# Kernel tuning notes

Measured on AMD Instinct MI355X. Metric: run time of the kernel, lower is better.

## Reference

```python
import jax, jax.numpy as jnp
import numpy as np

PH, PW = 7, 7
SPATIAL_SCALE = 0.0625


def _hat_int(t):
    # Antiderivative of the unit hat (triangle) function phi(t)=max(0,1-|t|),
    # i.e. integral_{-inf}^{t} phi. Piecewise quadratic, saturates to [0,1].
    t = jnp.clip(t, -1.0, 1.0)
    return jnp.where(t <= 0, 0.5 * (t + 1.0) ** 2, 1.0 - 0.5 * (1.0 - t) ** 2)


def _bin_weights(lo, hi, size):
    # lo, hi: [R, P] continuous bin boundaries (in feature-map coordinates).
    # Returns [R, P, size]: exact 1D integral of the hat basis at each integer
    # grid node over [lo, hi]. Bilinear interpolation is the tensor product of
    # 1D hat bases, so the exact 2D PrRoI integral separates into these weights.
    grid = jnp.arange(size, dtype=lo.dtype)
    return _hat_int(hi[..., None] - grid) - _hat_int(lo[..., None] - grid)


def _prroi_pool(features, rois):
    N, C, H, W = features.shape
    R = rois.shape[0]
    dt = features.dtype
    bidx = rois[:, 0].astype(jnp.int32)
    x1 = rois[:, 1] * SPATIAL_SCALE
    y1 = rois[:, 2] * SPATIAL_SCALE
    x2 = rois[:, 3] * SPATIAL_SCALE
    y2 = rois[:, 4] * SPATIAL_SCALE
    roi_w = jnp.maximum(x2 - x1, 0.0)
    roi_h = jnp.maximum(y2 - y1, 0.0)
    bw = roi_w / PW  # [R]
    bh = roi_h / PH
    px = jnp.arange(PW, dtype=dt)
    py = jnp.arange(PH, dtype=dt)
    x_lo = x1[:, None] + px[None, :] * bw[:, None]  # [R, PW]
    x_hi = x_lo + bw[:, None]
    y_lo = y1[:, None] + py[None, :] * bh[:, None]  # [R, PH]
    y_hi = y_lo + bh[:, None]
    Wx = _bin_weights(x_lo, x_hi, W)  # [R, PW, W]
    Wy = _bin_weights(y_lo, y_hi, H)  # [R, PH, H]
    area = bw * bh  # [R]
    inv_area = jnp.where(area > 0, 1.0 / jnp.maximum(area, 1e-12), 0.0)
    out = jnp.zeros((R, C, PH, PW), dtype=dt)
    for n in range(N):  # small fixed batch loop; avoids [R,C,H,W] gather
        m = (bidx == n).astype(dt)
        out = out + jnp.einsum('rph,chw,rqw->rcpq', Wy * m[:, None, None], features[n], Wx)
    return out * inv_area[:, None, None, None]


def setup_inputs() -> dict:
    key = jax.random.key(0)
    k1, k2, k3, k4, k5, k6 = jax.random.split(key, 6)
    N, C, H, W, R = 2, 256, 152, 152, 512
    features = jax.random.normal(k1, (N, C, H, W), dtype=jnp.float32)
    img = H / SPATIAL_SCALE  # 2432 px image
    bidx = jax.random.randint(k2, (R,), 0, N).astype(jnp.float32)
    x1 = jax.random.uniform(k3, (R,), minval=0.0, maxval=img * 0.7)
    y1 = jax.random.uniform(k4, (R,), minval=0.0, maxval=img * 0.7)
    x2 = x1 + jax.random.uniform(k5, (R,), minval=32.0, maxval=img * 0.3)
    y2 = y1 + jax.random.uniform(k6, (R,), minval=32.0, maxval=img * 0.3)
    rois = jnp.stack([bidx, x1, y1, x2, y2], axis=1).astype(jnp.float32)
    return {"features": features, "rois": rois}


def reference(features, rois):
    return _prroi_pool(features, rois)
```

## Files before the change

kernel.cpp:

```cpp
#include <hip/hip_runtime.h>

#define PHH 7
#define PWW 7
#define WXW 48
static constexpr float SPATIAL_SCALE = 0.0625f;

__device__ __forceinline__ float hat_int(float t) {
    t = fminf(fmaxf(t, -1.0f), 1.0f);
    float a = t + 1.0f, b = 1.0f - t;
    return (t <= 0.0f) ? 0.5f * a * a : 1.0f - 0.5f * b * b;
}

__device__ __forceinline__ float bin_w(float lo, float hi, float g) {
    return hat_int(hi - g) - hat_int(lo - g);
}

__device__ __forceinline__ unsigned short f32_to_bf16_rne(float x) {
    unsigned int u = __float_as_uint(x);
    unsigned int r = 0x7FFFu + ((u >> 16) & 1u);
    return (unsigned short)((u + r) >> 16);
}

__device__ __forceinline__ float bf_lo(unsigned int v) {
    return __uint_as_float(v << 16);
}
__device__ __forceinline__ float bf_hi(unsigned int v) {
    return __uint_as_float(v & 0xFFFF0000u);
}

__global__ __launch_bounds__(256) void transpose_weights(
    const float* __restrict__ src, unsigned short* __restrict__ dst,
    const float* __restrict__ rois, float* __restrict__ wx,
    float* __restrict__ wys, int C, int HW, int H, int W, int R)
{
    const int bid = (int)blockIdx.x +
                    (int)gridDim.x * ((int)blockIdx.y + (int)gridDim.y * (int)blockIdx.z);
    const int tid = threadIdx.x;
    if (bid < R && tid < 112) {
        const float* roi = rois + (size_t)bid * 5;
        const float x1 = roi[1] * SPATIAL_SCALE;
        const float y1 = roi[2] * SPATIAL_SCALE;
        const float x2 = roi[3] * SPATIAL_SCALE;
        const float y2 = roi[4] * SPATIAL_SCALE;
        const float bw = fmaxf(x2 - x1, 0.0f) / (float)PWW;
        const float bh = fmaxf(y2 - y1, 0.0f) / (float)PHH;
        const float area = bw * bh;
        const float inv_area = (area > 0.0f) ? 1.0f / fmaxf(area, 1e-12f) : 0.0f;
        if (tid < WXW) {
            const int w0 = max(0, (int)ceilf(x1 - 1.0f));
            const int w1 = min(W - 1, (int)floorf(x2 + 1.0f));
            const int ww = min(w1 - w0 + 1, WXW);
            const float g = (float)(w0 + tid);
            float* o = wx + ((size_t)bid * WXW + tid) * 8;
            #pragma unroll
            for (int q = 0; q < PWW; ++q) {
                const float lo = x1 + (float)q * bw;
                o[q] = (tid < ww) ? bin_w(lo, lo + bw, g) * inv_area : 0.0f;
            }
            o[7] = 0.0f;
        }
        {
            const int p = tid >> 4;
            const int i = tid & 15;
            const float ylo = y1 + (float)p * bh;
            const float yhi = ylo + bh;
            const int h0 = max(0, (int)ceilf(ylo - 1.0f));
            const int h1 = min(H - 1, (int)floorf(yhi + 1.0f));
            const int nh = min(h1 - h0 + 1, 16);
            wys[((size_t)bid * PHH + p) * 16 + i] =
                (i < nh) ? bin_w(ylo, yhi, (float)(h0 + i)) : 0.0f;
        }
    }

    __shared__ unsigned short tile[64][66];
    const int n = blockIdx.z;
    const int hw0 = blockIdx.x * 64;
    const int c0 = blockIdx.y * 64;
    const float* s = src + (size_t)n * C * HW;
    unsigned short* d = dst + (size_t)n * C * HW;

    const int tx = threadIdx.x & 63;
    const int ty = threadIdx.x >> 6;
    #pragma unroll
    for (int i = 0; i < 16; ++i) {
        const int cl = ty * 16 + i;
        const int c = c0 + cl, hw = hw0 + tx;
        if (c < C && hw < HW)
            tile[cl][tx] = f32_to_bf16_rne(s[(size_t)c * HW + hw]);
    }
    __syncthreads();

    const int cl = threadIdx.x & 31;
    const int hb = threadIdx.x >> 5;
    #pragma unroll
    for (int i = 0; i < 8; ++i) {
        const int hwl = hb * 8 + i;
        const int hw = hw0 + hwl;
        const int c = c0 + 2 * cl;
        if (hw < HW && c < C) {
            const unsigned int v = (unsigned int)tile[2 * cl][hwl]
                                 | ((unsigned int)tile[2 * cl + 1][hwl] << 16);
            *(unsigned int*)(d + (size_t)hw * C + c) = v;
        }
    }
}

__global__ __launch_bounds__(128, 4) void prroi_pool_nolds(
    const unsigned short* __restrict__ ft,
    const float* __restrict__ rois,
    const float* __restrict__ wx,
    const float* __restrict__ wys,
    float* __restrict__ out,
    int H, int W, int R)
{
    const int nwg = R * PHH;
    int task = (int)blockIdx.x;
    if ((nwg & 7) == 0) {
        const int cpx = nwg >> 3;
        task = (task & 7) * cpx + (task >> 3);
    }
    const int r = task / PHH;
    const int p = task % PHH;

    const int chHalf = threadIdx.x >> 6;
    const int lane = threadIdx.x & 63;
    const int c0 = chHalf * 128 + lane * 2;

    const float* roi = rois + (size_t)r * 5;
    const int b = (int)roi[0];
    const float x1 = roi[1] * SPATIAL_SCALE;
    const float y1 = roi[2] * SPATIAL_SCALE;
    const float x2 = roi[3] * SPATIAL_SCALE;
    const float y2 = roi[4] * SPATIAL_SCALE;
    const float bh = fmaxf(y2 - y1, 0.0f) / (float)PHH;

    const float ylo = y1 + (float)p * bh;
    const float yhi = ylo + bh;
    const int h0 = max(0, (int)ceilf(ylo - 1.0f));
    const int h1 = min(H - 1, (int)floorf(yhi + 1.0f));
    const int w0 = max(0, (int)ceilf(x1 - 1.0f));
    const int w1 = min(W - 1, (int)floorf(x2 + 1.0f));
    const int nh = min(h1 - h0 + 1, 16);
    const int nh4 = (nh + 3) & ~3;
    const int ww = min(w1 - w0 + 1, WXW);

    const float* wysr = wys + ((size_t)r * PHH + p) * 16;
    const float* wxr = wx + (size_t)r * WXW * 8;

    float acc[PWW][2];
    #pragma unroll
    for (int q = 0; q < PWW; ++q) { acc[q][0] = 0.0f; acc[q][1] = 0.0f; }

    const size_t rowstride = (size_t)W * 256;
    const unsigned short* base =
        ft + ((size_t)b * H + (size_t)h0) * rowstride + (size_t)w0 * 256 + c0;
    const int nhm1 = nh - 1;

    for (int chunk = 0; chunk < ww; chunk += 8) {
        int off[8];
        #pragma unroll
        for (int j = 0; j < 8; ++j)
            off[j] = (chunk + j < ww) ? (chunk + j) * 256 : 0;

        float u[2][8];
        #pragma unroll
        for (int j = 0; j < 8; ++j) { u[0][j] = 0.0f; u[1][j] = 0.0f; }

        for (int i = 0; i < nh4; i += 4) {
            unsigned int v[4][8];
            #pragma unroll
            for (int k = 0; k < 4; ++k) {
                const unsigned short* rp = base + (size_t)min(i + k, nhm1) * rowstride;
                #pragma unroll
                for (int j = 0; j < 8; ++j)
                    v[k][j] = *(const unsigned int*)(rp + off[j]);
            }
            #pragma unroll
            for (int k = 0; k < 4; ++k) {
                const float wy = wysr[i + k];
                #pragma unroll
                for (int j = 0; j < 8; ++j) {
                    u[0][j] = fmaf(wy, bf_lo(v[k][j]), u[0][j]);
                    u[1][j] = fmaf(wy, bf_hi(v[k][j]), u[1][j]);
                }
            }
        }

        #pragma unroll
        for (int j = 0; j < 8; ++j) {
            const float4 wa = *(const float4*)&wxr[(chunk + j) * 8];
            const float4 wb = *(const float4*)&wxr[(chunk + j) * 8 + 4];
            acc[0][0] = fmaf(wa.x, u[0][j], acc[0][0]);
            acc[0][1] = fmaf(wa.x, u[1][j], acc[0][1]);
            acc[1][0] = fmaf(wa.y, u[0][j], acc[1][0]);
            acc[1][1] = fmaf(wa.y, u[1][j], acc[1][1]);
            acc[2][0] = fmaf(wa.z, u[0][j], acc[2][0]);
            acc[2][1] = fmaf(wa.z, u[1][j], acc[2][1]);
            acc[3][0] = fmaf(wa.w, u[0][j], acc[3][0]);
            acc[3][1] = fmaf(wa.w, u[1][j], acc[3][1]);
            acc[4][0] = fmaf(wb.x, u[0][j], acc[4][0]);
            acc[4][1] = fmaf(wb.x, u[1][j], acc[4][1]);
            acc[5][0] = fmaf(wb.y, u[0][j], acc[5][0]);
            acc[5][1] = fmaf(wb.y, u[1][j], acc[5][1]);
            acc[6][0] = fmaf(wb.z, u[0][j], acc[6][0]);
            acc[6][1] = fmaf(wb.z, u[1][j], acc[6][1]);
        }
    }

    float* o = out + ((size_t)r * 256 + c0) * (PHH * PWW) + p * PWW;
    #pragma unroll
    for (int q = 0; q < PWW; ++q) {
        o[q]             = acc[q][0];
        o[PHH * PWW + q] = acc[q][1];
    }
}

__global__ __launch_bounds__(256) void prroi_pool_nchw(
    const float* __restrict__ f, const float* __restrict__ rois,
    float* __restrict__ out, int C, int H, int W, int R)
{
    const int idx = blockIdx.x * blockDim.x + threadIdx.x;
    const int total = R * C * PHH * PWW;
    if (idx >= total) return;
    const int q = idx % PWW;
    const int p = (idx / PWW) % PHH;
    const int c = (idx / (PWW * PHH)) % C;
    const int r = idx / (PWW * PHH * C);
    const float* roi = rois + (size_t)r * 5;
    const int b = (int)roi[0];
    const float x1 = roi[1] * SPATIAL_SCALE;
    const float y1 = roi[2] * SPATIAL_SCALE;
    const float x2 = roi[3] * SPATIAL_SCALE;
    const float y2 = roi[4] * SPATIAL_SCALE;
    const float bw = fmaxf(x2 - x1, 0.0f) / (float)PWW;
    const float bh = fmaxf(y2 - y1, 0.0f) / (float)PHH;
    const float area = bw * bh;
    const float inv_area = (area > 0.0f) ? 1.0f / fmaxf(area, 1e-12f) : 0.0f;
    const float xlo = x1 + (float)q * bw, xhi = xlo + bw;
    const float ylo = y1 + (float)p * bh, yhi = ylo + bh;
    const int h0 = max(0, (int)ceilf(ylo - 1.0f));
    const int h1 = min(H - 1, (int)floorf(yhi + 1.0f));
    const int w0 = max(0, (int)ceilf(xlo - 1.0f));
    const int w1 = min(W - 1, (int)floorf(xhi + 1.0f));
    float acc = 0.0f;
    for (int h = h0; h <= h1; ++h) {
        const float wy = bin_w(ylo, yhi, (float)h);
        const float* fr = f + (((size_t)b * C + c) * H + h) * W;
        for (int w = w0; w <= w1; ++w)
            acc = fmaf(wy * bin_w(xlo, xhi, (float)w), fr[w], acc);
    }
    out[idx] = acc * inv_area;
}

extern "C" void kernel_launch(void* const* d_in, const int* in_sizes, int n_in,
                              void* d_out, int out_size, void* d_ws, size_t ws_size,
                              hipStream_t stream)
{
    const float* features = (const float*)d_in[0];
    const float* rois = (const float*)d_in[1];
    float* out = (float*)d_out;

    const int C = 256, H = 152, W = 152;
    const int N = in_sizes[0] / (C * H * W);
    const int R = in_sizes[1] / 5;

    const size_t ft_bytes = (size_t)N * C * H * W * sizeof(unsigned short);
    const size_t wx_off = ft_bytes;
    const size_t wys_off = wx_off + (size_t)R * WXW * 8 * 4;
    const size_t need = wys_off + (size_t)R * PHH * 16 * 4;

    if (ws_size >= need && C == 256) {
        unsigned short* ft = (unsigned short*)d_ws;
        float* wx = (float*)((char*)d_ws + wx_off);
        float* wys = (float*)((char*)d_ws + wys_off);
        const int HW = H * W;
        dim3 tgrid((HW + 63) / 64, (C + 63) / 64, N);
        transpose_weights<<<tgrid, 256, 0, stream>>>(
            features, ft, rois, wx, wys, C, HW, H, W, R);
        prroi_pool_nolds<<<R * PHH, 128, 0, stream>>>(ft, rois, wx, wys, out, H, W, R);
    } else {
        const int total = R * C * PHH * PWW;
        prroi_pool_nchw<<<(total + 255) / 256, 256, 0, stream>>>(features, rois, out, C, H, W, R);
    }
}
```

Measured before the change: 56.05 us.

## Stream feature tiles into LDS via async global_load_lds double buffering

Replaces the direct register loads of bf16 feature rows with direct global-to-LDS DMA loads into a per-wave double-buffered ring. The next 4x8 tile is issued before the current one is consumed, and explicit vmcnt waits let memory latency overlap the FMA work while cutting register pressure. It adds 32KB of shared memory per block and drops the occupancy hint, which may reduce resident blocks. Correctness depends on the hand-written vmcnt counting matching the number of issued loads, and on no barrier being needed because each wave only reads its own slab.

```diff
diff --git a/kernel.cpp b/kernel.cpp
--- a/kernel.cpp
+++ b/kernel.cpp
@@ -26,6 +26,13 @@
 }
 __device__ __forceinline__ float bf_hi(unsigned int v) {
     return __uint_as_float(v & 0xFFFF0000u);
+}
+
+__device__ __forceinline__ void gload_lds4(const unsigned short* g, void* lds) {
+    __builtin_amdgcn_global_load_lds(
+        (const __attribute__((address_space(1))) unsigned int*)g,
+        (__attribute__((address_space(3))) unsigned int*)lds,
+        4, 0, 0);
 }
 
 __global__ __launch_bounds__(256) void transpose_weights(
@@ -105,7 +112,7 @@
     }
 }
 
-__global__ __launch_bounds__(128, 4) void prroi_pool_nolds(
+__global__ __launch_bounds__(128) void prroi_pool_dma(
     const unsigned short* __restrict__ ft,
     const float* __restrict__ rois,
     const float* __restrict__ wx,
@@ -147,6 +154,9 @@
     const float* wysr = wys + ((size_t)r * PHH + p) * 16;
     const float* wxr = wx + (size_t)r * WXW * 8;
 
+    __shared__ unsigned int slab[2][2][2048];
+    unsigned int (*sl)[2048] = slab[chHalf];
+
     float acc[PWW][2];
     #pragma unroll
     for (int q = 0; q < PWW; ++q) { acc[q][0] = 0.0f; acc[q][1] = 0.0f; }
@@ -155,41 +165,57 @@
     const unsigned short* base =
         ft + ((size_t)b * H + (size_t)h0) * rowstride + (size_t)w0 * 256 + c0;
     const int nhm1 = nh - 1;
-
-    for (int chunk = 0; chunk < ww; chunk += 8) {
-        int off[8];
+    const int nchunks = (ww + 7) >> 3;
+    const int nrq = nh4 >> 2;
+    const int ntiles = nchunks * nrq;
+
+    auto issue = [&](int c, int rq, int ring) {
         #pragma unroll
-        for (int j = 0; j < 8; ++j)
-            off[j] = (chunk + j < ww) ? (chunk + j) * 256 : 0;
-
+        for (int k = 0; k < 4; ++k) {
+            const int row = min(rq * 4 + k, nhm1);
+            const unsigned short* rp = base + (size_t)row * rowstride;
+            #pragma unroll
+            for (int j = 0; j < 8; ++j) {
+                const int col = c * 8 + j;
+                const int off = (col < ww) ? col * 256 : 0;
+                gload_lds4(rp + off, &sl[ring][(k * 8 + j) * 64]);
+            }
+        }
+    };
+
+    issue(0, 0, 0);
+    int t = 0;
+    for (int c = 0; c < nchunks; ++c) {
         float u[2][8];
         #pragma unroll
         for (int j = 0; j < 8; ++j) { u[0][j] = 0.0f; u[1][j] = 0.0f; }
 
-        for (int i = 0; i < nh4; i += 4) {
-            unsigned int v[4][8];
-            #pragma unroll
-            for (int k = 0; k < 4; ++k) {
-                const unsigned short* rp = base + (size_t)min(i + k, nhm1) * rowstride;
-                #pragma unroll
-                for (int j = 0; j < 8; ++j)
-                    v[k][j] = *(const unsigned int*)(rp + off[j]);
+        for (int rq = 0; rq < nrq; ++rq, ++t) {
+            const int ring = t & 1;
+            if (t + 1 < ntiles) {
+                int cn = c, rqn = rq + 1;
+                if (rqn == nrq) { cn = c + 1; rqn = 0; }
+                issue(cn, rqn, (t + 1) & 1);
+                asm volatile("s_waitcnt vmcnt(32)" ::: "memory");
+            } else {
+                asm volatile("s_waitcnt vmcnt(0)" ::: "memory");
             }
             #pragma unroll
             for (int k = 0; k < 4; ++k) {
-                const float wy = wysr[i + k];
+                const float wy = wysr[rq * 4 + k];
                 #pragma unroll
                 for (int j = 0; j < 8; ++j) {
-                    u[0][j] = fmaf(wy, bf_lo(v[k][j]), u[0][j]);
-                    u[1][j] = fmaf(wy, bf_hi(v[k][j]), u[1][j]);
+                    const unsigned int v = sl[ring][(k * 8 + j) * 64 + lane];
+                    u[0][j] = fmaf(wy, bf_lo(v), u[0][j]);
+                    u[1][j] = fmaf(wy, bf_hi(v), u[1][j]);
                 }
             }
         }
 
         #pragma unroll
         for (int j = 0; j < 8; ++j) {
-            const float4 wa = *(const float4*)&wxr[(chunk + j) * 8];
-            const float4 wb = *(const float4*)&wxr[(chunk + j) * 8 + 4];
+            const float4 wa = *(const float4*)&wxr[(c * 8 + j) * 8];
+            const float4 wb = *(const float4*)&wxr[(c * 8 + j) * 8 + 4];
             acc[0][0] = fmaf(wa.x, u[0][j], acc[0][0]);
             acc[0][1] = fmaf(wa.x, u[1][j], acc[0][1]);
             acc[1][0] = fmaf(wa.y, u[0][j], acc[1][0]);
@@ -277,7 +303,7 @@
         dim3 tgrid((HW + 63) / 64, (C + 63) / 64, N);
         transpose_weights<<<tgrid, 256, 0, stream>>>(
             features, ft, rois, wx, wys, C, HW, H, W, R);
-        prroi_pool_nolds<<<R * PHH, 128, 0, stream>>>(ft, rois, wx, wys, out, H, W, R);
+        prroi_pool_dma<<<R * PHH, 128, 0, stream>>>(ft, rois, wx, wys, out, H, W, R);
     } else {
         const int total = R * C * PHH * PWW;
         prroi_pool_nchw<<<(total + 255) / 256, 256, 0, stream>>>(features, rois, out, C, H, W, R);
```

After: 70.19 us. 25.2% more time.

## Split column chunks across waves with 4-channel vector loads and LDS reduction

Applied to the files above, without the earlier changes.

Each thread now covers 4 channels with 8-byte loads instead of 2 channels with 4-byte loads, so one wave spans all 256 channels. The two waves of a block instead split the width chunks (alternating 8-column chunks) and combine their partial accumulators through shared memory before writing. This widens memory accesses and changes the parallel split, but it doubles register use for the accumulators and adds a sync plus an LDS reduction. Load imbalance between waves is possible when the number of columns is not a multiple of 16.

```diff
diff --git a/kernel.cpp b/kernel.cpp
--- a/kernel.cpp
+++ b/kernel.cpp
@@ -105,7 +105,7 @@
     }
 }
 
-__global__ __launch_bounds__(128, 4) void prroi_pool_nolds(
+__global__ __launch_bounds__(128, 4) void prroi_pool_u2(
     const unsigned short* __restrict__ ft,
     const float* __restrict__ rois,
     const float* __restrict__ wx,
@@ -122,9 +122,9 @@
     const int r = task / PHH;
     const int p = task % PHH;
 
-    const int chHalf = threadIdx.x >> 6;
+    const int colWave = threadIdx.x >> 6;
     const int lane = threadIdx.x & 63;
-    const int c0 = chHalf * 128 + lane * 2;
+    const int c0 = lane * 4;
 
     const float* roi = rois + (size_t)r * 5;
     const int b = (int)roi[0];
@@ -141,47 +141,55 @@
     const int w0 = max(0, (int)ceilf(x1 - 1.0f));
     const int w1 = min(W - 1, (int)floorf(x2 + 1.0f));
     const int nh = min(h1 - h0 + 1, 16);
-    const int nh4 = (nh + 3) & ~3;
+    const int nh2 = (nh + 1) & ~1;
     const int ww = min(w1 - w0 + 1, WXW);
 
     const float* wysr = wys + ((size_t)r * PHH + p) * 16;
     const float* wxr = wx + (size_t)r * WXW * 8;
 
-    float acc[PWW][2];
+    __shared__ float rbuf[64 * 29];
+
+    float acc[PWW][4];
     #pragma unroll
-    for (int q = 0; q < PWW; ++q) { acc[q][0] = 0.0f; acc[q][1] = 0.0f; }
+    for (int q = 0; q < PWW; ++q)
+        #pragma unroll
+        for (int ch = 0; ch < 4; ++ch) acc[q][ch] = 0.0f;
 
     const size_t rowstride = (size_t)W * 256;
     const unsigned short* base =
         ft + ((size_t)b * H + (size_t)h0) * rowstride + (size_t)w0 * 256 + c0;
     const int nhm1 = nh - 1;
 
-    for (int chunk = 0; chunk < ww; chunk += 8) {
+    for (int chunk = colWave * 8; chunk < ww; chunk += 16) {
         int off[8];
         #pragma unroll
         for (int j = 0; j < 8; ++j)
             off[j] = (chunk + j < ww) ? (chunk + j) * 256 : 0;
 
-        float u[2][8];
-        #pragma unroll
-        for (int j = 0; j < 8; ++j) { u[0][j] = 0.0f; u[1][j] = 0.0f; }
-
-        for (int i = 0; i < nh4; i += 4) {
-            unsigned int v[4][8];
-            #pragma unroll
-            for (int k = 0; k < 4; ++k) {
+        float u[4][8];
+        #pragma unroll
+        for (int ch = 0; ch < 4; ++ch)
+            #pragma unroll
+            for (int j = 0; j < 8; ++j) u[ch][j] = 0.0f;
+
+        for (int i = 0; i < nh2; i += 2) {
+            uint2 v[2][8];
+            #pragma unroll
+            for (int k = 0; k < 2; ++k) {
                 const unsigned short* rp = base + (size_t)min(i + k, nhm1) * rowstride;
                 #pragma unroll
                 for (int j = 0; j < 8; ++j)
-                    v[k][j] = *(const unsigned int*)(rp + off[j]);
+                    v[k][j] = *(const uint2*)(rp + off[j]);
             }
             #pragma unroll
-            for (int k = 0; k < 4; ++k) {
+            for (int k = 0; k < 2; ++k) {
                 const float wy = wysr[i + k];
                 #pragma unroll
                 for (int j = 0; j < 8; ++j) {
-                    u[0][j] = fmaf(wy, bf_lo(v[k][j]), u[0][j]);
-                    u[1][j] = fmaf(wy, bf_hi(v[k][j]), u[1][j]);
+                    u[0][j] = fmaf(wy, bf_lo(v[k][j].x), u[0][j]);
+                    u[1][j] = fmaf(wy, bf_hi(v[k][j].x), u[1][j]);
+                    u[2][j] = fmaf(wy, bf_lo(v[k][j].y), u[2][j]);
+                    u[3][j] = fmaf(wy, bf_hi(v[k][j].y), u[3][j]);
                 }
             }
         }
@@ -190,28 +198,35 @@
         for (int j = 0; j < 8; ++j) {
             const float4 wa = *(const float4*)&wxr[(chunk + j) * 8];
             const float4 wb = *(const float4*)&wxr[(chunk + j) * 8 + 4];
-            acc[0][0] = fmaf(wa.x, u[0][j], acc[0][0]);
-            acc[0][1] = fmaf(wa.x, u[1][j], acc[0][1]);
-            acc[1][0] = fmaf(wa.y, u[0][j], acc[1][0]);
-            acc[1][1] = fmaf(wa.y, u[1][j], acc[1][1]);
-            acc[2][0] = fmaf(wa.z, u[0][j], acc[2][0]);
-            acc[2][1] = fmaf(wa.z, u[1][j], acc[2][1]);
-            acc[3][0] = fmaf(wa.w, u[0][j], acc[3][0]);
-            acc[3][1] = fmaf(wa.w, u[1][j], acc[3][1]);
-            acc[4][0] = fmaf(wb.x, u[0][j], acc[4][0]);
-            acc[4][1] = fmaf(wb.x, u[1][j], acc[4][1]);
-            acc[5][0] = fmaf(wb.y, u[0][j], acc[5][0]);
-            acc[5][1] = fmaf(wb.y, u[1][j], acc[5][1]);
-            acc[6][0] = fmaf(wb.z, u[0][j], acc[6][0]);
-            acc[6][1] = fmaf(wb.z, u[1][j], acc[6][1]);
-        }
-    }
-
-    float* o = out + ((size_t)r * 256 + c0) * (PHH * PWW) + p * PWW;
-    #pragma unroll
-    for (int q = 0; q < PWW; ++q) {
-        o[q]             = acc[q][0];
-        o[PHH * PWW + q] = acc[q][1];
+            #pragma unroll
+            for (int ch = 0; ch < 4; ++ch) {
+                acc[0][ch] = fmaf(wa.x, u[ch][j], acc[0][ch]);
+                acc[1][ch] = fmaf(wa.y, u[ch][j], acc[1][ch]);
+                acc[2][ch] = fmaf(wa.z, u[ch][j], acc[2][ch]);
+                acc[3][ch] = fmaf(wa.w, u[ch][j], acc[3][ch]);
+                acc[4][ch] = fmaf(wb.x, u[ch][j], acc[4][ch]);
+                acc[5][ch] = fmaf(wb.y, u[ch][j], acc[5][ch]);
+                acc[6][ch] = fmaf(wb.z, u[ch][j], acc[6][ch]);
+            }
+        }
+    }
+
+    float* pbuf = rbuf + lane * 29;
+    if (colWave == 1) {
+        #pragma unroll
+        for (int q = 0; q < PWW; ++q)
+            #pragma unroll
+            for (int ch = 0; ch < 4; ++ch)
+                pbuf[q * 4 + ch] = acc[q][ch];
+    }
+    __syncthreads();
+    if (colWave == 0) {
+        float* o = out + ((size_t)r * 256 + c0) * (PHH * PWW) + p * PWW;
+        #pragma unroll
+        for (int ch = 0; ch < 4; ++ch)
+            #pragma unroll
+            for (int q = 0; q < PWW; ++q)
+                o[(size_t)ch * (PHH * PWW) + q] = acc[q][ch] + pbuf[q * 4 + ch];
     }
 }
 
@@ -277,7 +292,7 @@
         dim3 tgrid((HW + 63) / 64, (C + 63) / 64, N);
         transpose_weights<<<tgrid, 256, 0, stream>>>(
             features, ft, rois, wx, wys, C, HW, H, W, R);
-        prroi_pool_nolds<<<R * PHH, 128, 0, stream>>>(ft, rois, wx, wys, out, H, W, R);
+        prroi_pool_u2<<<R * PHH, 128, 0, stream>>>(ft, rois, wx, wys, out, H, W, R);
     } else {
         const int total = R * C * PHH * PWW;
         prroi_pool_nchw<<<(total + 255) / 256, 256, 0, stream>>>(features, rois, out, C, H, W, R);
```

Measured after the change: 73.40 us. 1.31x slower.
